# Kernel optimization log

Measured on AMD Instinct MI355X. Metric: run time of the kernel, lower is better.

Reference implementation:

```python
import jax, jax.numpy as jnp
import numpy as np

# Model hyperparameters (match init_kwargs / module defaults)
B, P, F_IN, H, K, OUT = 1024, 256, 8, 16, 8, 1


def _lin_init(key, out_f, in_f, bias=True):
    # torch nn.Linear default: U(-1/sqrt(in), 1/sqrt(in))
    kw, kb = jax.random.split(key)
    bound = 1.0 / np.sqrt(in_f)
    W = jax.random.uniform(kw, (out_f, in_f), jnp.float32, -bound, bound)
    if bias:
        b = jax.random.uniform(kb, (out_f,), jnp.float32, -bound, bound)
        return W, b
    return W


def setup_inputs() -> dict:
    key = jax.random.key(0)
    ks = jax.random.split(key, 7)
    x = jax.random.normal(ks[0], (B, P * F_IN), jnp.float32)
    W1 = _lin_init(ks[1], H, F_IN, bias=False)          # part_encode[0], bias=False
    W2, b2 = _lin_init(ks[2], H, H)                      # part_encode[2]
    W3, b3 = _lin_init(ks[3], H, H)                      # part_encode[4]
    We, be = _lin_init(ks[4], H, 2 * H)                  # edge MLP Linear(2H, H)
    Wo1, bo1 = _lin_init(ks[5], H // 2, H)               # output[0]
    Wo2, bo2 = _lin_init(ks[6], OUT, H // 2)             # output[2]
    return {"x": x, "W1": W1, "W2": W2, "b2": b2, "W3": W3, "b3": b3,
            "We": We, "be": be, "Wo1": Wo1, "bo1": bo1, "Wo2": Wo2, "bo2": bo2}


def reference(x, W1, W2, b2, W3, b3, We, be, Wo1, bo1, Wo2, bo2):
    b = x.shape[0]
    # part_encode MLP on flattened particles
    h = x.reshape(b * P, F_IN)
    h = jax.nn.elu(h @ W1.T)
    h = jax.nn.elu(h @ W2.T + b2)
    h = jax.nn.elu(h @ W3.T + b3)
    h = h.reshape(b, P, H)                               # [B,P,H]

    # Dynamic kNN graph per batch element (knn includes self at distance 0,
    # matching torch_cluster.knn on identical query/source sets)
    sq = jnp.sum(h * h, axis=-1)                         # [B,P]
    dist = sq[:, :, None] + sq[:, None, :] - 2.0 * jnp.einsum('bid,bjd->bij', h, h)
    _, idx = jax.lax.top_k(-dist, K)                     # [B,P,K] nearest neighbors

    # Gather neighbor features per graph
    xj = jax.vmap(lambda hb, ib: hb[ib])(h, idx)         # [B,P,K,H]
    xi = jnp.broadcast_to(h[:, :, None, :], xj.shape)    # [B,P,K,H]
    edge = jnp.concatenate([xi, xj - xi], axis=-1)       # [B,P,K,2H]

    # Edge MLP + max aggregation (EdgeConv message nn([x_i, x_j - x_i]), aggr='max')
    m = jax.nn.elu(edge @ We.T + be)                     # [B,P,K,H]
    node = jnp.max(m, axis=2)                            # [B,P,H]

    # avg_pool_x over nodes of each graph
    pooled = jnp.mean(node, axis=1)                      # [B,H]

    # output MLP + sigmoid (act_out=True, batchnorm=False)
    o = jax.nn.elu(pooled @ Wo1.T + bo1)
    o = o @ Wo2.T + bo2
    return jax.nn.sigmoid(o)                             # [B,OUT]
```

## Files before the change

### kernel.cpp

```cpp
#include <hip/hip_runtime.h>
#include <math.h>

#define NB 1024
#define NP 256
#define FIN 8
#define NH 16
#define NK 8

#define REP8A(X)  X(0) X(1) X(2) X(3) X(4) X(5) X(6) X(7)
#define REP16A(X) X(0) X(1) X(2) X(3) X(4) X(5) X(6) X(7) X(8) X(9) X(10) X(11) X(12) X(13) X(14) X(15)
#define REP16B(X) X(0) X(1) X(2) X(3) X(4) X(5) X(6) X(7) X(8) X(9) X(10) X(11) X(12) X(13) X(14) X(15)

typedef short s8v __attribute__((ext_vector_type(8)));
typedef float f4v __attribute__((ext_vector_type(4)));
typedef unsigned int u4v __attribute__((ext_vector_type(4)));

__device__ __forceinline__ float elu_f(float v) {
    return v > 0.f ? v : (__expf(v) - 1.f);
}
__device__ __forceinline__ unsigned bf16r(float f) {
    unsigned u = __float_as_uint(f);
    return (u + 0x7FFFu + ((u >> 16) & 1u)) >> 16;
}
__device__ __forceinline__ float ush2f(unsigned short u) {
    return __uint_as_float(((unsigned)u) << 16);
}

#define CE(a, b) { float lo_ = fminf(a, b), hi_ = fmaxf(a, b); a = lo_; b = hi_; }
#define SORT8(x0,x1,x2,x3,x4,x5,x6,x7) \
    CE(x0,x1) CE(x2,x3) CE(x4,x5) CE(x6,x7) \
    CE(x0,x2) CE(x1,x3) CE(x4,x6) CE(x5,x7) \
    CE(x1,x2) CE(x5,x6) \
    CE(x0,x4) CE(x1,x5) CE(x2,x6) CE(x3,x7) \
    CE(x2,x4) CE(x3,x5) \
    CE(x1,x2) CE(x3,x4) CE(x5,x6)
#define MERGE8(x0,x1,x2,x3,x4,x5,x6,x7) \
    R0 = fminf(R0, x7); R1 = fminf(R1, x6); R2 = fminf(R2, x5); R3 = fminf(R3, x4); \
    R4 = fminf(R4, x3); R5 = fminf(R5, x2); R6 = fminf(R6, x1); R7 = fminf(R7, x0); \
    CE(R0,R4) CE(R1,R5) CE(R2,R6) CE(R3,R7) \
    CE(R0,R2) CE(R1,R3) CE(R4,R6) CE(R5,R7) \
    CE(R0,R1) CE(R2,R3) CE(R4,R5) CE(R6,R7)

__global__ __attribute__((amdgpu_flat_work_group_size(256, 256),
                          amdgpu_waves_per_eu(2, 4)))
void edgenet_kernel(
    const float* __restrict__ gx,
    const float* __restrict__ gW1, const float* __restrict__ gW2, const float* __restrict__ gb2,
    const float* __restrict__ gW3, const float* __restrict__ gb3,
    const float* __restrict__ gWe, const float* __restrict__ gbe,
    const float* __restrict__ gWo1, const float* __restrict__ gbo1,
    const float* __restrict__ gWo2, const float* __restrict__ gbo2,
    float* __restrict__ gout)
{
    const int b  = blockIdx.x;
    const int t  = threadIdx.x;
    const int w  = t >> 6;
    const int lq = (t >> 4) & 3;
    const int lc = t & 15;

    __shared__ __align__(16) unsigned short hF[16][4][136];
    __shared__ __align__(16) float sq2arr[256];
    __shared__ __align__(16) float spanel[4][64][20];
    __shared__ float spool[64];

    float xi0, xi1, xi2, xi3, xi4, xi5, xi6, xi7;
    {
        const float4* xr = reinterpret_cast<const float4*>(gx + (size_t)b * (NP * FIN) + t * FIN);
        float4 v0 = xr[0], v1 = xr[1];
        xi0 = v0.x; xi1 = v0.y; xi2 = v0.z; xi3 = v0.w;
        xi4 = v1.x; xi5 = v1.y; xi6 = v1.z; xi7 = v1.w;
    }

    float l1_0,l1_1,l1_2,l1_3,l1_4,l1_5,l1_6,l1_7,l1_8,l1_9,l1_10,l1_11,l1_12,l1_13,l1_14,l1_15;
    float l2_0,l2_1,l2_2,l2_3,l2_4,l2_5,l2_6,l2_7,l2_8,l2_9,l2_10,l2_11,l2_12,l2_13,l2_14,l2_15;
    float hp0,hp1,hp2,hp3,hp4,hp5,hp6,hp7,hp8,hp9,hp10,hp11,hp12,hp13,hp14,hp15;

#define L1_BODY(i) s = fmaf(gW1[(o_) * FIN + i], xi##i, s);
#define L1_O(o) { const int o_ = (o); float s = 0.f; REP8A(L1_BODY) l1_##o = elu_f(s); }
    REP16A(L1_O)
#undef L1_O
#undef L1_BODY
#define L2_BODY(i) s = fmaf(gW2[(o_) * NH + i], l1_##i, s);
#define L2_O(o) { const int o_ = (o); float s = gb2[o_]; REP16B(L2_BODY) l2_##o = elu_f(s); }
    REP16A(L2_O)
#undef L2_O
#undef L2_BODY
#define L3_BODY(i) s = fmaf(gW3[(o_) * NH + i], l2_##i, s);
#define L3_O(o) { const int o_ = (o); float s = gb3[o_]; REP16B(L3_BODY) hp##o = elu_f(s); }
    REP16A(L3_O)
#undef L3_O
#undef L3_BODY

    float base0,base1,base2,base3,base4,base5,base6,base7,
          base8,base9,base10,base11,base12,base13,base14,base15;
#define BAS_BODY(i) s = fmaf(gWe[(o_) * 32 + i] - gWe[(o_) * 32 + 16 + i], hp##i, s);
#define BAS_O(o) { const int o_ = (o); float s = gbe[o_]; REP16B(BAS_BODY) base##o = s; }
    REP16A(BAS_O)
#undef BAS_O
#undef BAS_BODY

    s8v eB1;
    {
        float4 wv = *reinterpret_cast<const float4*>(gWe + lc * 32 + 16 + 4 * lq);
        unsigned h0 = bf16r(wv.x), h1 = bf16r(wv.y), h2 = bf16r(wv.z), h3 = bf16r(wv.w);
        unsigned g0 = bf16r(wv.x - ush2f((unsigned short)h0));
        unsigned g1 = bf16r(wv.y - ush2f((unsigned short)h1));
        unsigned g2 = bf16r(wv.z - ush2f((unsigned short)h2));
        unsigned g3 = bf16r(wv.w - ush2f((unsigned short)h3));
        eB1 = (s8v){(short)h0, (short)h1, (short)h2, (short)h3,
                    (short)g0, (short)g1, (short)g2, (short)g3};
    }

    float sqp = 0.f;
#define SQ_I(i) sqp = fmaf(hp##i, hp##i, sqp);
    REP16A(SQ_I)
#undef SQ_I
    const float sqp2 = 0.5f * sqp;

#define PACKQ(q, A, B, C, D) { \
    unsigned ha = bf16r(hp##A), hb = bf16r(hp##B), hc = bf16r(hp##C), hd = bf16r(hp##D); \
    float ra = hp##A - ush2f((unsigned short)ha); \
    float rb = hp##B - ush2f((unsigned short)hb); \
    float rc = hp##C - ush2f((unsigned short)hc); \
    float rd = hp##D - ush2f((unsigned short)hd); \
    unsigned la = bf16r(ra), lb = bf16r(rb), lcc = bf16r(rc), ld = bf16r(rd); \
    u4v pk; pk.x = ha | (hb << 16); pk.y = hc | (hd << 16); \
            pk.z = la | (lb << 16); pk.w = lcc | (ld << 16); \
    *(u4v*)&hF[t >> 4][q][(t & 15) * 8] = pk; }
    PACKQ(0, 0, 1, 2, 3)
    PACKQ(1, 4, 5, 6, 7)
    PACKQ(2, 8, 9, 10, 11)
    PACKQ(3, 12, 13, 14, 15)
#undef PACKQ
    sq2arr[t] = sqp2;
    __syncthreads();

    const s8v af0 = *(const s8v*)&hF[4 * w + 0][lq][lc * 8];
    const s8v af1 = *(const s8v*)&hF[4 * w + 1][lq][lc * 8];
    const s8v af2 = *(const s8v*)&hF[4 * w + 2][lq][lc * 8];
    const s8v af3 = *(const s8v*)&hF[4 * w + 3][lq][lc * 8];

    float R0, R1, R2, R3, R4, R5, R6, R7;
    R0=R1=R2=R3=R4=R5=R6=R7 = __uint_as_float(0x7F7FFFFFu);

    for (int jt = 0; jt < 16; ++jt) {
        const s8v bf1 = *(const s8v*)&hF[jt][lq][lc * 8];
        const s8v bf2 = __builtin_shufflevector(bf1, bf1, 4, 5, 6, 7, 0, 1, 2, 3);
        const float4 sqv = *(const float4*)&sq2arr[16 * jt + 4 * lq];
        f4v z = {0.f, 0.f, 0.f, 0.f};
#define GRAM_T(tt) { \
        f4v ac = __builtin_amdgcn_mfma_f32_16x16x32_bf16(bf1, af##tt, z, 0, 0, 0); \
        ac     = __builtin_amdgcn_mfma_f32_16x16x32_bf16(bf2, af##tt, ac, 0, 0, 0); \
        float4 ov; ov.x = sqv.x - ac[0]; ov.y = sqv.y - ac[1]; \
                   ov.z = sqv.z - ac[2]; ov.w = sqv.w - ac[3]; \
        *(float4*)&spanel[w][16 * (tt) + lc][4 * lq] = ov; }
        GRAM_T(0) GRAM_T(1) GRAM_T(2) GRAM_T(3)
#undef GRAM_T

        const float4* pr = (const float4*)&spanel[w][t & 63][0];
        const float4 q0 = pr[0], q1 = pr[1], q2 = pr[2], q3 = pr[3];
        const int jt16 = jt * 16;
#define KEY(c, val) __uint_as_float((__float_as_uint((val) + sqp2) & 0xFFFFFF00u) | (unsigned)(jt16 + (c)))
        float k0  = KEY(0,  q0.x), k1  = KEY(1,  q0.y);
        float k2  = KEY(2,  q0.z), k3  = KEY(3,  q0.w);
        float k4  = KEY(4,  q1.x), k5  = KEY(5,  q1.y);
        float k6  = KEY(6,  q1.z), k7  = KEY(7,  q1.w);
        float k8  = KEY(8,  q2.x), k9  = KEY(9,  q2.y);
        float k10 = KEY(10, q2.z), k11 = KEY(11, q2.w);
        float k12 = KEY(12, q3.x), k13 = KEY(13, q3.y);
        float k14 = KEY(14, q3.z), k15 = KEY(15, q3.w);
#undef KEY
        SORT8(k0, k1, k2, k3, k4, k5, k6, k7)
        SORT8(k8, k9, k10, k11, k12, k13, k14, k15)
        MERGE8(k0, k1, k2, k3, k4, k5, k6, k7)
        MERGE8(k8, k9, k10, k11, k12, k13, k14, k15)
    }

    float* sbase = &spanel[w][0][0];
    uint2* jj    = (uint2*)(&spanel[w][0][0] + 1088);
    {
        unsigned idxlo = (__float_as_uint(R0) & 0xFFu)
                       | ((__float_as_uint(R1) & 0xFFu) << 8)
                       | ((__float_as_uint(R2) & 0xFFu) << 16)
                       | ((__float_as_uint(R3) & 0xFFu) << 24);
        unsigned idxhi = (__float_as_uint(R4) & 0xFFu)
                       | ((__float_as_uint(R5) & 0xFFu) << 8)
                       | ((__float_as_uint(R6) & 0xFFu) << 16)
                       | ((__float_as_uint(R7) & 0xFFu) << 24);
        jj[t & 63] = make_uint2(idxlo, idxhi);
    }
    {
        float* sb = sbase + (t & 63) * 17;
#define SBW(i) sb[i] = base##i;
        REP16A(SBW)
#undef SBW
    }

    float psum = 0.f;
    {
        const s8v eB2 = __builtin_shufflevector(eB1, eB1, 4, 5, 6, 7, 0, 1, 2, 3);
        const int erow = lc;
        #pragma unroll 4
        for (int tt = 0; tt < 32; ++tt) {
            uint2 jv = jj[2 * tt + (erow >> 3)];
            unsigned word = (erow & 4) ? jv.y : jv.x;
            int jp = (int)((word >> ((erow & 3) * 8)) & 0xFFu);
            const s8v av = *(const s8v*)&hF[jp >> 4][lq][(jp & 15) * 8];
            f4v z = {0.f, 0.f, 0.f, 0.f};
            f4v d1 = __builtin_amdgcn_mfma_f32_16x16x32_bf16(av, eB1, z, 0, 0, 0);
            d1     = __builtin_amdgcn_mfma_f32_16x16x32_bf16(av, eB2, d1, 0, 0, 0);
            float mx = fmaxf(fmaxf(d1[0], d1[1]), fmaxf(d1[2], d1[3]));
            mx = fmaxf(mx, __shfl_xor(mx, 16, 64));
            float bz = sbase[(2 * tt + (lq >> 1)) * 17 + lc];
            psum += elu_f(mx + bz);
        }
    }
    psum += __shfl_xor(psum, 16, 64);
    psum += __shfl_xor(psum, 32, 64);
    if ((t & 63) < 16) spool[(w << 4) + lc] = psum;
    __syncthreads();

    if (t == 0) {
#define PL(i) const float pl##i = (spool[i] + spool[16 + i] + spool[32 + i] + spool[48 + i]) * (1.f / 512.f);
        REP16A(PL)
#undef PL
        float o1_0,o1_1,o1_2,o1_3,o1_4,o1_5,o1_6,o1_7;
#define HD_BODY(i) s = fmaf(gWo1[(o_) * NH + i], pl##i, s);
#define HD_O(o) { const int o_ = (o); float s = gbo1[o_]; REP16B(HD_BODY) o1_##o = elu_f(s); }
        REP8A(HD_O)
#undef HD_O
#undef HD_BODY
        float o2 = gbo2[0];
        o2 = fmaf(gWo2[0], o1_0, o2); o2 = fmaf(gWo2[1], o1_1, o2);
        o2 = fmaf(gWo2[2], o1_2, o2); o2 = fmaf(gWo2[3], o1_3, o2);
        o2 = fmaf(gWo2[4], o1_4, o2); o2 = fmaf(gWo2[5], o1_5, o2);
        o2 = fmaf(gWo2[6], o1_6, o2); o2 = fmaf(gWo2[7], o1_7, o2);
        gout[b] = 1.f / (1.f + expf(-o2));
    }
}

extern "C" void kernel_launch(void* const* d_in, const int* in_sizes, int n_in,
                              void* d_out, int out_size, void* d_ws, size_t ws_size,
                              hipStream_t stream) {
    const float* x   = (const float*)d_in[0];
    const float* W1  = (const float*)d_in[1];
    const float* W2  = (const float*)d_in[2];
    const float* b2  = (const float*)d_in[3];
    const float* W3  = (const float*)d_in[4];
    const float* b3  = (const float*)d_in[5];
    const float* We  = (const float*)d_in[6];
    const float* be  = (const float*)d_in[7];
    const float* Wo1 = (const float*)d_in[8];
    const float* bo1 = (const float*)d_in[9];
    const float* Wo2 = (const float*)d_in[10];
    const float* bo2 = (const float*)d_in[11];
    float* out = (float*)d_out;

    hipLaunchKernelGGL(edgenet_kernel, dim3(NB), dim3(NP), 0, stream,
                       x, W1, W2, b2, W3, b3, We, be, Wo1, bo1, Wo2, bo2, out);
}
```

Measured before the change: 143.6 us.

## Select kNN directly from MFMA output fragments, dropping LDS panel transpose

The kNN selection now works straight on the MFMA accumulator registers, with no round trip through an LDS panel. Each lane handles one query tile at a time and keeps a partial top-8 over the columns it owns. The four lanes' partial results are then merged with cross-lane shuffles. The edge-stage base values are written straight to shared memory instead of staying in registers, and the index list gets its own array. This removes the per-iteration LDS store/load transposes, at the cost of four sequential passes with extra MFMAs (the B fragments are reloaded per query tile) and shuffle-merge networks.

```diff
diff --git a/kernel.cpp b/kernel.cpp
--- a/kernel.cpp
+++ b/kernel.cpp
@@ -40,6 +40,59 @@
     CE(R0,R4) CE(R1,R5) CE(R2,R6) CE(R3,R7) \
     CE(R0,R2) CE(R1,R3) CE(R4,R6) CE(R5,R7) \
     CE(R0,R1) CE(R2,R3) CE(R4,R5) CE(R6,R7)
+
+#define KEYV(val, c) __uint_as_float((__float_as_uint((val) + sqp2) & 0xFFFFFF00u) | (unsigned)(c))
+
+#define KNN_TT(ttc) { \
+    const s8v af = *(const s8v*)&hF[4 * w + (ttc)][lq][lc * 8]; \
+    float R0, R1, R2, R3, R4, R5, R6, R7; \
+    R0=R1=R2=R3=R4=R5=R6=R7 = __uint_as_float(0x7F7FFFFFu); \
+    for (int jt2 = 0; jt2 < 8; ++jt2) { \
+        const s8v b1a = *(const s8v*)&hF[2 * jt2][lq][lc * 8]; \
+        const s8v b1b = *(const s8v*)&hF[2 * jt2 + 1][lq][lc * 8]; \
+        const s8v b2a = __builtin_shufflevector(b1a, b1a, 4, 5, 6, 7, 0, 1, 2, 3); \
+        const s8v b2b = __builtin_shufflevector(b1b, b1b, 4, 5, 6, 7, 0, 1, 2, 3); \
+        const float4 sqa = *(const float4*)&sq2arr[32 * jt2 + 4 * lq]; \
+        const float4 sqb = *(const float4*)&sq2arr[32 * jt2 + 16 + 4 * lq]; \
+        f4v z = {0.f, 0.f, 0.f, 0.f}; \
+        f4v a1 = __builtin_amdgcn_mfma_f32_16x16x32_bf16(b1a, af, z, 0, 0, 0); \
+        f4v a2 = __builtin_amdgcn_mfma_f32_16x16x32_bf16(b2a, af, z, 0, 0, 0); \
+        f4v a3 = __builtin_amdgcn_mfma_f32_16x16x32_bf16(b1b, af, z, 0, 0, 0); \
+        f4v a4 = __builtin_amdgcn_mfma_f32_16x16x32_bf16(b2b, af, z, 0, 0, 0); \
+        const int c0 = 32 * jt2 + 4 * lq, c1 = c0 + 16; \
+        float k0 = KEYV(sqa.x - a1[0] - a2[0], c0 + 0); \
+        float k1 = KEYV(sqa.y - a1[1] - a2[1], c0 + 1); \
+        float k2 = KEYV(sqa.z - a1[2] - a2[2], c0 + 2); \
+        float k3 = KEYV(sqa.w - a1[3] - a2[3], c0 + 3); \
+        float k4 = KEYV(sqb.x - a3[0] - a4[0], c1 + 0); \
+        float k5 = KEYV(sqb.y - a3[1] - a4[1], c1 + 1); \
+        float k6 = KEYV(sqb.z - a3[2] - a4[2], c1 + 2); \
+        float k7 = KEYV(sqb.w - a3[3] - a4[3], c1 + 3); \
+        SORT8(k0, k1, k2, k3, k4, k5, k6, k7) \
+        MERGE8(k0, k1, k2, k3, k4, k5, k6, k7) \
+    } \
+    { float o0 = __shfl_xor(R0, 16), o1 = __shfl_xor(R1, 16), \
+            o2 = __shfl_xor(R2, 16), o3 = __shfl_xor(R3, 16), \
+            o4 = __shfl_xor(R4, 16), o5 = __shfl_xor(R5, 16), \
+            o6 = __shfl_xor(R6, 16), o7 = __shfl_xor(R7, 16); \
+      MERGE8(o0, o1, o2, o3, o4, o5, o6, o7) } \
+    { float o0 = __shfl_xor(R0, 32), o1 = __shfl_xor(R1, 32), \
+            o2 = __shfl_xor(R2, 32), o3 = __shfl_xor(R3, 32), \
+            o4 = __shfl_xor(R4, 32), o5 = __shfl_xor(R5, 32), \
+            o6 = __shfl_xor(R6, 32), o7 = __shfl_xor(R7, 32); \
+      MERGE8(o0, o1, o2, o3, o4, o5, o6, o7) } \
+    if (lq == (ttc)) { \
+        unsigned plo = (__float_as_uint(R0) & 0xFFu) \
+                     | ((__float_as_uint(R1) & 0xFFu) << 8) \
+                     | ((__float_as_uint(R2) & 0xFFu) << 16) \
+                     | ((__float_as_uint(R3) & 0xFFu) << 24); \
+        unsigned phi = (__float_as_uint(R4) & 0xFFu) \
+                     | ((__float_as_uint(R5) & 0xFFu) << 8) \
+                     | ((__float_as_uint(R6) & 0xFFu) << 16) \
+                     | ((__float_as_uint(R7) & 0xFFu) << 24); \
+        jjarr[w][16 * (ttc) + lc] = make_uint2(plo, phi); \
+    } \
+}
 
 __global__ __attribute__((amdgpu_flat_work_group_size(256, 256),
                           amdgpu_waves_per_eu(2, 4)))
@@ -60,7 +113,8 @@
 
     __shared__ __align__(16) unsigned short hF[16][4][136];
     __shared__ __align__(16) float sq2arr[256];
-    __shared__ __align__(16) float spanel[4][64][20];
+    __shared__ __align__(16) float sbaseA[4][64][17];
+    __shared__ __align__(16) uint2 jjarr[4][64];
     __shared__ float spool[64];
 
     float xi0, xi1, xi2, xi3, xi4, xi5, xi6, xi7;
@@ -91,13 +145,14 @@
 #undef L3_O
 #undef L3_BODY
 
-    float base0,base1,base2,base3,base4,base5,base6,base7,
-          base8,base9,base10,base11,base12,base13,base14,base15;
+    {
+        float* sb = &sbaseA[w][t & 63][0];
 #define BAS_BODY(i) s = fmaf(gWe[(o_) * 32 + i] - gWe[(o_) * 32 + 16 + i], hp##i, s);
-#define BAS_O(o) { const int o_ = (o); float s = gbe[o_]; REP16B(BAS_BODY) base##o = s; }
-    REP16A(BAS_O)
+#define BAS_O(o) { const int o_ = (o); float s = gbe[o_]; REP16B(BAS_BODY) sb[o_] = s; }
+        REP16A(BAS_O)
 #undef BAS_O
 #undef BAS_BODY
+    }
 
     s8v eB1;
     {
@@ -135,66 +190,10 @@
     sq2arr[t] = sqp2;
     __syncthreads();
 
-    const s8v af0 = *(const s8v*)&hF[4 * w + 0][lq][lc * 8];
-    const s8v af1 = *(const s8v*)&hF[4 * w + 1][lq][lc * 8];
-    const s8v af2 = *(const s8v*)&hF[4 * w + 2][lq][lc * 8];
-    const s8v af3 = *(const s8v*)&hF[4 * w + 3][lq][lc * 8];
-
-    float R0, R1, R2, R3, R4, R5, R6, R7;
-    R0=R1=R2=R3=R4=R5=R6=R7 = __uint_as_float(0x7F7FFFFFu);
-
-    for (int jt = 0; jt < 16; ++jt) {
-        const s8v bf1 = *(const s8v*)&hF[jt][lq][lc * 8];
-        const s8v bf2 = __builtin_shufflevector(bf1, bf1, 4, 5, 6, 7, 0, 1, 2, 3);
-        const float4 sqv = *(const float4*)&sq2arr[16 * jt + 4 * lq];
-        f4v z = {0.f, 0.f, 0.f, 0.f};
-#define GRAM_T(tt) { \
-        f4v ac = __builtin_amdgcn_mfma_f32_16x16x32_bf16(bf1, af##tt, z, 0, 0, 0); \
-        ac     = __builtin_amdgcn_mfma_f32_16x16x32_bf16(bf2, af##tt, ac, 0, 0, 0); \
-        float4 ov; ov.x = sqv.x - ac[0]; ov.y = sqv.y - ac[1]; \
-                   ov.z = sqv.z - ac[2]; ov.w = sqv.w - ac[3]; \
-        *(float4*)&spanel[w][16 * (tt) + lc][4 * lq] = ov; }
-        GRAM_T(0) GRAM_T(1) GRAM_T(2) GRAM_T(3)
-#undef GRAM_T
-
-        const float4* pr = (const float4*)&spanel[w][t & 63][0];
-        const float4 q0 = pr[0], q1 = pr[1], q2 = pr[2], q3 = pr[3];
-        const int jt16 = jt * 16;
-#define KEY(c, val) __uint_as_float((__float_as_uint((val) + sqp2) & 0xFFFFFF00u) | (unsigned)(jt16 + (c)))
-        float k0  = KEY(0,  q0.x), k1  = KEY(1,  q0.y);
-        float k2  = KEY(2,  q0.z), k3  = KEY(3,  q0.w);
-        float k4  = KEY(4,  q1.x), k5  = KEY(5,  q1.y);
-        float k6  = KEY(6,  q1.z), k7  = KEY(7,  q1.w);
-        float k8  = KEY(8,  q2.x), k9  = KEY(9,  q2.y);
-        float k10 = KEY(10, q2.z), k11 = KEY(11, q2.w);
-        float k12 = KEY(12, q3.x), k13 = KEY(13, q3.y);
-        float k14 = KEY(14, q3.z), k15 = KEY(15, q3.w);
-#undef KEY
-        SORT8(k0, k1, k2, k3, k4, k5, k6, k7)
-        SORT8(k8, k9, k10, k11, k12, k13, k14, k15)
-        MERGE8(k0, k1, k2, k3, k4, k5, k6, k7)
-        MERGE8(k8, k9, k10, k11, k12, k13, k14, k15)
-    }
-
-    float* sbase = &spanel[w][0][0];
-    uint2* jj    = (uint2*)(&spanel[w][0][0] + 1088);
-    {
-        unsigned idxlo = (__float_as_uint(R0) & 0xFFu)
-                       | ((__float_as_uint(R1) & 0xFFu) << 8)
-                       | ((__float_as_uint(R2) & 0xFFu) << 16)
-                       | ((__float_as_uint(R3) & 0xFFu) << 24);
-        unsigned idxhi = (__float_as_uint(R4) & 0xFFu)
-                       | ((__float_as_uint(R5) & 0xFFu) << 8)
-                       | ((__float_as_uint(R6) & 0xFFu) << 16)
-                       | ((__float_as_uint(R7) & 0xFFu) << 24);
-        jj[t & 63] = make_uint2(idxlo, idxhi);
-    }
-    {
-        float* sb = sbase + (t & 63) * 17;
-#define SBW(i) sb[i] = base##i;
-        REP16A(SBW)
-#undef SBW
-    }
+    KNN_TT(0)
+    KNN_TT(1)
+    KNN_TT(2)
+    KNN_TT(3)
 
     float psum = 0.f;
     {
@@ -202,7 +201,7 @@
         const int erow = lc;
         #pragma unroll 4
         for (int tt = 0; tt < 32; ++tt) {
-            uint2 jv = jj[2 * tt + (erow >> 3)];
+            uint2 jv = jjarr[w][2 * tt + (erow >> 3)];
             unsigned word = (erow & 4) ? jv.y : jv.x;
             int jp = (int)((word >> ((erow & 3) * 8)) & 0xFFu);
             const s8v av = *(const s8v*)&hF[jp >> 4][lq][(jp & 15) * 8];
@@ -211,7 +210,7 @@
             d1     = __builtin_amdgcn_mfma_f32_16x16x32_bf16(av, eB2, d1, 0, 0, 0);
             float mx = fmaxf(fmaxf(d1[0], d1[1]), fmaxf(d1[2], d1[3]));
             mx = fmaxf(mx, __shfl_xor(mx, 16, 64));
-            float bz = sbase[(2 * tt + (lq >> 1)) * 17 + lc];
+            float bz = sbaseA[w][2 * tt + (lq >> 1)][lc];
             psum += elu_f(mx + bz);
         }
     }
```

After: 131.5 us. 8.4% less time.
